# Kernel tuning notes

Measured on AMD Instinct MI355X. Metric: run time of the kernel, lower is better.

Reference implementation:

```python
import jax, jax.numpy as jnp
import numpy as np

B, S, HID = 2, 2048, 2304
H, KVH, D = 8, 4, 256          # query heads, kv heads, head_dim
N_REP = H // KVH
SCALE = 256.0 ** -0.5          # query_pre_attn_scalar ** -0.5
SOFTCAP = 50.0
ROPE_THETA = 10000.0
NEG = -1e9


def setup_inputs() -> dict:
    key = jax.random.key(0)
    k1, k2, k3, k4, k5 = jax.random.split(key, 5)
    hidden_states = jax.random.normal(k1, (B, S, HID), dtype=jnp.float32)
    # RoPE cos/sin tables, shape [B, S, D]
    inv_freq = 1.0 / (ROPE_THETA ** (jnp.arange(0, D, 2, dtype=jnp.float32) / D))
    pos = jnp.arange(S, dtype=jnp.float32)
    freqs = pos[:, None] * inv_freq[None, :]            # [S, D/2]
    emb = jnp.concatenate([freqs, freqs], axis=-1)      # [S, D]
    cos = jnp.broadcast_to(jnp.cos(emb)[None], (B, S, D))
    sin = jnp.broadcast_to(jnp.sin(emb)[None], (B, S, D))
    # additive causal mask [B, 1, S, S] (sliding_window=4096 > S, so pure causal)
    idx = jnp.arange(S)
    causal = idx[None, :] <= idx[:, None]
    attention_mask = jnp.broadcast_to(
        jnp.where(causal, 0.0, NEG).astype(jnp.float32)[None, None], (B, 1, S, S))
    # projection weights (lecun-normal-ish scale), no bias (attention_bias=False)
    Wq = jax.random.normal(k2, (HID, H * D), dtype=jnp.float32) / np.sqrt(HID)
    Wk = jax.random.normal(k3, (HID, KVH * D), dtype=jnp.float32) / np.sqrt(HID)
    Wv = jax.random.normal(k4, (HID, KVH * D), dtype=jnp.float32) / np.sqrt(HID)
    Wo = jax.random.normal(k5, (H * D, HID), dtype=jnp.float32) / np.sqrt(H * D)
    return {"hidden_states": hidden_states, "cos": cos, "sin": sin,
            "attention_mask": attention_mask,
            "Wq": Wq, "Wk": Wk, "Wv": Wv, "Wo": Wo}


def _rotate_half(x):
    half = x.shape[-1] // 2
    return jnp.concatenate([-x[..., half:], x[..., :half]], axis=-1)


def reference(hidden_states, cos, sin, attention_mask, Wq, Wk, Wv, Wo):
    b, s, _ = hidden_states.shape
    q = (hidden_states @ Wq).reshape(b, s, H, D).transpose(0, 2, 1, 3)    # [B,H,S,D]
    k = (hidden_states @ Wk).reshape(b, s, KVH, D).transpose(0, 2, 1, 3)  # [B,KVH,S,D]
    v = (hidden_states @ Wv).reshape(b, s, KVH, D).transpose(0, 2, 1, 3)
    c = cos[:, None]  # [B,1,S,D] broadcast over heads (unsqueeze_dim=1)
    sn = sin[:, None]
    q = q * c + _rotate_half(q) * sn
    k = k * c + _rotate_half(k) * sn
    # GQA: repeat kv heads (interleave, matching repeat_kv tile+reshape)
    k = jnp.repeat(k, N_REP, axis=1)
    v = jnp.repeat(v, N_REP, axis=1)
    w = jnp.einsum('bhqd,bhkd->bhqk', q, k) * SCALE
    w = jnp.tanh(w / SOFTCAP) * SOFTCAP                  # logit softcapping
    w = w + attention_mask[:, :, :, :s]
    w = jax.nn.softmax(w.astype(jnp.float32), axis=-1).astype(q.dtype)
    out = jnp.einsum('bhqk,bhkd->bhqd', w, v)
    out = out.transpose(0, 2, 1, 3).reshape(b, s, H * D)
    return out @ Wo
```

## Files before the change

### kernel.cpp

```cpp
#include <hip/hip_runtime.h>

typedef unsigned short u16;
typedef __attribute__((ext_vector_type(8))) short short8;
typedef __attribute__((ext_vector_type(4))) float f32x4;

constexpr int B_ = 2;
constexpr int H_ = 8;
constexpr int KVH_ = 4;
constexpr int S_ = 2048;
constexpr int D_ = 256;
constexpr int HID_ = 2304;
constexpr int QKVN_ = 4096;
constexpr int AON_ = 2048;

__device__ __forceinline__ float b2f(u16 u) {
  union { float f; unsigned int i; } x; x.i = ((unsigned int)u) << 16; return x.f;
}
__device__ __forceinline__ u16 f2b(float f) {
  unsigned int x = __float_as_uint(f);
  unsigned int r = (x + 0x7fffu + ((x >> 16) & 1u)) >> 16;
  return (u16)r;
}

__global__ void cast_kernel(const float* __restrict__ in, u16* __restrict__ out) {
  size_t i = ((size_t)blockIdx.x * 256 + threadIdx.x) * 4;
  float4 v = *(const float4*)(in + i);
  unsigned int lo = (unsigned int)f2b(v.x) | ((unsigned int)f2b(v.y) << 16);
  unsigned int hi = (unsigned int)f2b(v.z) | ((unsigned int)f2b(v.w) << 16);
  uint2 o; o.x = lo; o.y = hi;
  *(uint2*)(out + i) = o;
}

__global__ void transpose_cast(const float* __restrict__ src, u16* __restrict__ dst,
                               int R, int C) {
  __shared__ float tile[64][65];
  int r0 = blockIdx.y * 64, c0 = blockIdx.x * 64;
  int t = threadIdx.x;
#pragma unroll
  for (int i = 0; i < 16; ++i) {
    int e = i * 256 + t;
    int r = e >> 6, c = e & 63;
    tile[r][c] = src[(size_t)(r0 + r) * C + (c0 + c)];
  }
  __syncthreads();
#pragma unroll
  for (int i = 0; i < 16; ++i) {
    int e = i * 256 + t;
    int orow = e >> 6, ocol = e & 63;
    dst[(size_t)(c0 + orow) * R + (r0 + ocol)] = f2b(tile[ocol][orow]);
  }
}

template <int OUTF32>
__global__ __launch_bounds__(256, 2) void gemm_bt(
    const u16* __restrict__ A, const u16* __restrict__ B, void* __restrict__ Cp,
    int M, int N, int K) {
  __shared__ u16 As[128 * 32];
  __shared__ u16 Bs[128 * 32];
  int m0 = blockIdx.y * 128, n0 = blockIdx.x * 128;
  int tid = threadIdx.x;
  int lane = tid & 63, wave = tid >> 6;
  int wy = wave >> 1, wx = wave & 1;
  int quad = lane >> 4, l16 = lane & 15;
  f32x4 acc[4][4] = {};
  for (int k0 = 0; k0 < K; k0 += 32) {
#pragma unroll
    for (int i = 0; i < 2; ++i) {
      int chunk = i * 256 + tid;
      int row = chunk >> 2, col = (chunk & 3) << 3;
      __builtin_amdgcn_global_load_lds(
          (const __attribute__((address_space(1))) void*)(A + (size_t)(m0 + row) * K + k0 + col),
          (__attribute__((address_space(3))) void*)(As + chunk * 8), 16, 0, 0);
    }
#pragma unroll
    for (int i = 0; i < 2; ++i) {
      int chunk = i * 256 + tid;
      int row = chunk >> 2, col = (chunk & 3) << 3;
      __builtin_amdgcn_global_load_lds(
          (const __attribute__((address_space(1))) void*)(B + (size_t)(n0 + row) * K + k0 + col),
          (__attribute__((address_space(3))) void*)(Bs + chunk * 8), 16, 0, 0);
    }
    __syncthreads();
    short8 af[4], bf[4];
#pragma unroll
    for (int mi = 0; mi < 4; ++mi)
      af[mi] = *(const short8*)(As + (wy * 64 + mi * 16 + l16) * 32 + quad * 8);
#pragma unroll
    for (int ni = 0; ni < 4; ++ni)
      bf[ni] = *(const short8*)(Bs + (wx * 64 + ni * 16 + l16) * 32 + quad * 8);
#pragma unroll
    for (int mi = 0; mi < 4; ++mi)
#pragma unroll
      for (int ni = 0; ni < 4; ++ni)
        acc[mi][ni] = __builtin_amdgcn_mfma_f32_16x16x32_bf16(af[mi], bf[ni], acc[mi][ni], 0, 0, 0);
    __syncthreads();
  }
#pragma unroll
  for (int mi = 0; mi < 4; ++mi) {
#pragma unroll
    for (int ni = 0; ni < 4; ++ni) {
#pragma unroll
      for (int r = 0; r < 4; ++r) {
        int row = m0 + wy * 64 + mi * 16 + quad * 4 + r;
        int col = n0 + wx * 64 + ni * 16 + l16;
        if (OUTF32)
          ((float*)Cp)[(size_t)row * N + col] = acc[mi][ni][r];
        else
          ((u16*)Cp)[(size_t)row * N + col] = f2b(acc[mi][ni][r]);
      }
    }
  }
}

__global__ void rope_kernel(const u16* __restrict__ qkv, const float* __restrict__ cs,
                            const float* __restrict__ sn, u16* __restrict__ Qr,
                            u16* __restrict__ Kr) {
  int row = blockIdx.x;
  int b = row >> 11, s = row & 2047;
  int d = threadIdx.x;
  const u16* qrow = qkv + (size_t)row * QKVN_;
  float c = cs[(size_t)row * D_ + d];
  float si = sn[(size_t)row * D_ + d];
  int dp = (d < 128) ? d + 128 : d - 128;
  float sgn = (d < 128) ? -1.f : 1.f;
#pragma unroll
  for (int h = 0; h < H_; ++h) {
    float v = b2f(qrow[h * D_ + d]);
    float p = sgn * b2f(qrow[h * D_ + dp]);
    Qr[((size_t)(b * H_ + h) * S_ + s) * D_ + d] = f2b(v * c + p * si);
  }
#pragma unroll
  for (int g = 0; g < KVH_; ++g) {
    float v = b2f(qrow[2048 + g * D_ + d]);
    float p = sgn * b2f(qrow[2048 + g * D_ + dp]);
    Kr[((size_t)(b * KVH_ + g) * S_ + s) * D_ + d] = f2b(v * c + p * si);
  }
}

__global__ void transpose_v(const u16* __restrict__ qkv, u16* __restrict__ Vt) {
  __shared__ u16 tile[64][72];
  int d0 = blockIdx.x * 64, s0 = blockIdx.y * 64, g = blockIdx.z;
  int b = g >> 2, kvh = g & 3;
  int t = threadIdx.x;
#pragma unroll
  for (int i = 0; i < 16; ++i) {
    int e = i * 256 + t;
    int r = e >> 6, c = e & 63;
    tile[r][c] = qkv[(size_t)(b * S_ + s0 + r) * QKVN_ + 3072 + kvh * D_ + d0 + c];
  }
  __syncthreads();
#pragma unroll
  for (int i = 0; i < 16; ++i) {
    int e = i * 256 + t;
    int orow = e >> 6, ocol = e & 63;
    Vt[((size_t)g * D_ + d0 + orow) * S_ + s0 + ocol] = tile[ocol][orow];
  }
}

__global__ __launch_bounds__(256, 2) void attn_kernel(
    const u16* __restrict__ Qr, const u16* __restrict__ Kr, const u16* __restrict__ Vt,
    u16* __restrict__ Ao) {
  __shared__ u16 Ks[32 * 256];
  __shared__ u16 Vs[256 * 32];
  __shared__ u16 Ps[4][16 * 40];
  int b = blockIdx.z;
  int qt = (b == 0) ? (31 - blockIdx.x) : blockIdx.x;
  int h = blockIdx.y;
  int kvh = h >> 1;
  int tid = threadIdx.x, wave = tid >> 6, lane = tid & 63;
  int quad = lane >> 4, l16 = lane & 15;
  int q0 = qt * 64;
  const u16* Qbase = Qr + ((size_t)(b * H_ + h) * S_ + q0 + wave * 16 + l16) * D_;
  short8 qf[8];
#pragma unroll
  for (int kk = 0; kk < 8; ++kk)
    qf[kk] = *(const short8*)(Qbase + kk * 32 + quad * 8);
  const u16* Kbase = Kr + (size_t)(b * KVH_ + kvh) * S_ * D_;
  const u16* Vbase = Vt + (size_t)(b * KVH_ + kvh) * D_ * S_;
  float l_r[4] = {0.f, 0.f, 0.f, 0.f};
  f32x4 o_acc[16] = {};
  int nkt = 2 * qt + 2;
  for (int kt = 0; kt < nkt; ++kt) {
    int k0 = kt * 32;
    __syncthreads();
#pragma unroll
    for (int i = 0; i < 4; ++i) {
      int p = i * 256 + tid;
      int s = p >> 5, pc = p & 31;
      int c = pc ^ (s & 7);
      __builtin_amdgcn_global_load_lds(
          (const __attribute__((address_space(1))) void*)(Kbase + (size_t)(k0 + s) * D_ + c * 8),
          (__attribute__((address_space(3))) void*)(Ks + p * 8), 16, 0, 0);
    }
#pragma unroll
    for (int i = 0; i < 4; ++i) {
      int p = i * 256 + tid;
      int d = p >> 2, ps = p & 3;
      int sl = ps ^ ((d >> 1) & 3);
      __builtin_amdgcn_global_load_lds(
          (const __attribute__((address_space(1))) void*)(Vbase + (size_t)d * S_ + k0 + sl * 8),
          (__attribute__((address_space(3))) void*)(Vs + p * 8), 16, 0, 0);
    }
    __syncthreads();
    f32x4 sacc[2] = {};
#pragma unroll
    for (int n = 0; n < 2; ++n) {
      int srow = n * 16 + l16;
      const u16* kb = Ks + srow * 256;
      int sw = l16 & 7;
#pragma unroll
      for (int kk = 0; kk < 8; ++kk) {
        int phys = (kk * 4 + quad) ^ sw;
        short8 bfr = *(const short8*)(kb + phys * 8);
        sacc[n] = __builtin_amdgcn_mfma_f32_16x16x32_bf16(qf[kk], bfr, sacc[n], 0, 0, 0);
      }
    }
    float rs[4] = {0.f, 0.f, 0.f, 0.f};
    bool full = (k0 + 31 <= q0 + wave * 16);
#pragma unroll
    for (int n = 0; n < 2; ++n) {
      int key = k0 + n * 16 + l16;
#pragma unroll
      for (int r = 0; r < 4; ++r) {
        float E = __expf(sacc[n][r] * 0.0025f);
        float ee = __expf(-100.0f * __frcp_rn(E + 1.0f));
        if (!full) {
          int qq = q0 + wave * 16 + quad * 4 + r;
          ee = (key <= qq) ? ee : 0.0f;
        }
        rs[r] += ee;
        Ps[wave][(quad * 4 + r) * 40 + n * 16 + l16] = f2b(ee);
      }
    }
#pragma unroll
    for (int off = 1; off < 16; off <<= 1)
#pragma unroll
      for (int r = 0; r < 4; ++r)
        rs[r] += __shfl_xor(rs[r], off, 64);
#pragma unroll
    for (int r = 0; r < 4; ++r) l_r[r] += rs[r];
    short8 pa = *(const short8*)(&Ps[wave][l16 * 40 + quad * 8]);
#pragma unroll
    for (int dt = 0; dt < 16; ++dt) {
      int d = dt * 16 + l16;
      int phys = quad ^ ((d >> 1) & 3);
      short8 vb = *(const short8*)(Vs + d * 32 + phys * 8);
      o_acc[dt] = __builtin_amdgcn_mfma_f32_16x16x32_bf16(pa, vb, o_acc[dt], 0, 0, 0);
    }
  }
#pragma unroll
  for (int r = 0; r < 4; ++r) l_r[r] = 1.0f / l_r[r];
#pragma unroll
  for (int dt = 0; dt < 16; ++dt)
#pragma unroll
    for (int r = 0; r < 4; ++r) {
      int row = b * S_ + q0 + wave * 16 + quad * 4 + r;
      int col = h * D_ + dt * 16 + l16;
      Ao[(size_t)row * AON_ + col] = f2b(o_acc[dt][r] * l_r[r]);
    }
}

extern "C" void kernel_launch(void* const* d_in, const int* in_sizes, int n_in,
                              void* d_out, int out_size, void* d_ws, size_t ws_size,
                              hipStream_t stream) {
  const float* hidden = (const float*)d_in[0];
  const float* cosp = (const float*)d_in[1];
  const float* sinp = (const float*)d_in[2];
  const float* Wq = (const float*)d_in[4];
  const float* Wk = (const float*)d_in[5];
  const float* Wv = (const float*)d_in[6];
  const float* Wo = (const float*)d_in[7];

  u16* hs  = (u16*)d_ws;
  u16* WT  = hs  + (size_t)4096 * HID_;
  u16* WoT = WT  + (size_t)4096 * HID_;
  u16* qkv = WoT + (size_t)HID_ * AON_;
  u16* Qr  = qkv + (size_t)4096 * QKVN_;
  u16* Kr  = Qr  + (size_t)B_ * H_ * S_ * D_;
  u16* Vt  = Kr  + (size_t)B_ * KVH_ * S_ * D_;
  u16* Ao  = Vt  + (size_t)B_ * KVH_ * S_ * D_;

  cast_kernel<<<9216, 256, 0, stream>>>(hidden, hs);
  transpose_cast<<<dim3(32, 36), 256, 0, stream>>>(Wq, WT, HID_, 2048);
  transpose_cast<<<dim3(16, 36), 256, 0, stream>>>(Wk, WT + (size_t)2048 * HID_, HID_, 1024);
  transpose_cast<<<dim3(16, 36), 256, 0, stream>>>(Wv, WT + (size_t)3072 * HID_, HID_, 1024);
  transpose_cast<<<dim3(36, 32), 256, 0, stream>>>(Wo, WoT, 2048, HID_);
  gemm_bt<0><<<dim3(32, 32), 256, 0, stream>>>(hs, WT, qkv, 4096, QKVN_, HID_);
  rope_kernel<<<4096, 256, 0, stream>>>(qkv, cosp, sinp, Qr, Kr);
  transpose_v<<<dim3(4, 32, 8), 256, 0, stream>>>(qkv, Vt);
  attn_kernel<<<dim3(32, 8, 2), 256, 0, stream>>>(Qr, Kr, Vt, Ao);
  gemm_bt<1><<<dim3(18, 32), 256, 0, stream>>>(Ao, WoT, d_out, 4096, HID_, 2048);
}
```

Before: 451.5 us.

## Double-buffer K/V LDS tiles and defer row-sum reduction to kernel end

The attention kernel now keeps two LDS buffers for K and V and issues the async global-to-LDS loads for the next key tile before computing on the current one. This overlaps memory latency with MFMA work and drops one barrier per iteration. The per-tile cross-lane shuffle reduction of the softmax row sums is replaced by per-lane partial sums reduced once after the loop. LDS use roughly doubles, which may limit occupancy at the requested two blocks per SM, and correctness relies on the trailing barrier ordering the buffer reuse.

```diff
diff --git a/kernel.cpp b/kernel.cpp
--- a/kernel.cpp
+++ b/kernel.cpp
@@ -160,8 +160,8 @@
 __global__ __launch_bounds__(256, 2) void attn_kernel(
     const u16* __restrict__ Qr, const u16* __restrict__ Kr, const u16* __restrict__ Vt,
     u16* __restrict__ Ao) {
-  __shared__ u16 Ks[32 * 256];
-  __shared__ u16 Vs[256 * 32];
+  __shared__ u16 Ks[2][32 * 256];
+  __shared__ u16 Vs[2][32 * 256];
   __shared__ u16 Ps[4][16 * 40];
   int b = blockIdx.z;
   int qt = (b == 0) ? (31 - blockIdx.x) : blockIdx.x;
@@ -177,36 +177,49 @@
     qf[kk] = *(const short8*)(Qbase + kk * 32 + quad * 8);
   const u16* Kbase = Kr + (size_t)(b * KVH_ + kvh) * S_ * D_;
   const u16* Vbase = Vt + (size_t)(b * KVH_ + kvh) * D_ * S_;
-  float l_r[4] = {0.f, 0.f, 0.f, 0.f};
+  int ksrc_s[4], ksrc_c[4], vsrc_d[4], vsrc_s[4];
+#pragma unroll
+  for (int i = 0; i < 4; ++i) {
+    int p = i * 256 + tid;
+    ksrc_s[i] = p >> 5;
+    ksrc_c[i] = (p & 31) ^ ((p >> 5) & 7);
+    vsrc_d[i] = p >> 2;
+    vsrc_s[i] = (p & 3) ^ ((p >> 3) & 3);
+  }
+  float lp[4] = {0.f, 0.f, 0.f, 0.f};
   f32x4 o_acc[16] = {};
   int nkt = 2 * qt + 2;
+
+#define STAGE(KT, BUF)                                                                   \
+  {                                                                                      \
+    int k0s = (KT) * 32;                                                                 \
+    _Pragma("unroll") for (int i = 0; i < 4; ++i) {                                      \
+      int p = i * 256 + tid;                                                             \
+      __builtin_amdgcn_global_load_lds(                                                  \
+          (const __attribute__((address_space(1))) void*)(Kbase +                        \
+              (size_t)(k0s + ksrc_s[i]) * D_ + ksrc_c[i] * 8),                           \
+          (__attribute__((address_space(3))) void*)(&Ks[BUF][0] + p * 8), 16, 0, 0);     \
+    }                                                                                    \
+    _Pragma("unroll") for (int i = 0; i < 4; ++i) {                                      \
+      int p = i * 256 + tid;                                                             \
+      __builtin_amdgcn_global_load_lds(                                                  \
+          (const __attribute__((address_space(1))) void*)(Vbase +                        \
+              (size_t)vsrc_d[i] * S_ + k0s + vsrc_s[i] * 8),                             \
+          (__attribute__((address_space(3))) void*)(&Vs[BUF][0] + p * 8), 16, 0, 0);     \
+    }                                                                                    \
+  }
+
+  STAGE(0, 0);
+  __syncthreads();
   for (int kt = 0; kt < nkt; ++kt) {
     int k0 = kt * 32;
-    __syncthreads();
-#pragma unroll
-    for (int i = 0; i < 4; ++i) {
-      int p = i * 256 + tid;
-      int s = p >> 5, pc = p & 31;
-      int c = pc ^ (s & 7);
-      __builtin_amdgcn_global_load_lds(
-          (const __attribute__((address_space(1))) void*)(Kbase + (size_t)(k0 + s) * D_ + c * 8),
-          (__attribute__((address_space(3))) void*)(Ks + p * 8), 16, 0, 0);
-    }
-#pragma unroll
-    for (int i = 0; i < 4; ++i) {
-      int p = i * 256 + tid;
-      int d = p >> 2, ps = p & 3;
-      int sl = ps ^ ((d >> 1) & 3);
-      __builtin_amdgcn_global_load_lds(
-          (const __attribute__((address_space(1))) void*)(Vbase + (size_t)d * S_ + k0 + sl * 8),
-          (__attribute__((address_space(3))) void*)(Vs + p * 8), 16, 0, 0);
-    }
-    __syncthreads();
+    int cur = kt & 1;
+    if (kt + 1 < nkt) STAGE(kt + 1, cur ^ 1);
     f32x4 sacc[2] = {};
 #pragma unroll
     for (int n = 0; n < 2; ++n) {
       int srow = n * 16 + l16;
-      const u16* kb = Ks + srow * 256;
+      const u16* kb = &Ks[cur][0] + srow * 256;
       int sw = l16 & 7;
 #pragma unroll
       for (int kk = 0; kk < 8; ++kk) {
@@ -215,7 +228,6 @@
         sacc[n] = __builtin_amdgcn_mfma_f32_16x16x32_bf16(qf[kk], bfr, sacc[n], 0, 0, 0);
       }
     }
-    float rs[4] = {0.f, 0.f, 0.f, 0.f};
     bool full = (k0 + 31 <= q0 + wave * 16);
 #pragma unroll
     for (int n = 0; n < 2; ++n) {
@@ -228,35 +240,35 @@
           int qq = q0 + wave * 16 + quad * 4 + r;
           ee = (key <= qq) ? ee : 0.0f;
         }
-        rs[r] += ee;
+        lp[r] += ee;
         Ps[wave][(quad * 4 + r) * 40 + n * 16 + l16] = f2b(ee);
       }
     }
-#pragma unroll
-    for (int off = 1; off < 16; off <<= 1)
-#pragma unroll
-      for (int r = 0; r < 4; ++r)
-        rs[r] += __shfl_xor(rs[r], off, 64);
-#pragma unroll
-    for (int r = 0; r < 4; ++r) l_r[r] += rs[r];
     short8 pa = *(const short8*)(&Ps[wave][l16 * 40 + quad * 8]);
 #pragma unroll
     for (int dt = 0; dt < 16; ++dt) {
       int d = dt * 16 + l16;
       int phys = quad ^ ((d >> 1) & 3);
-      short8 vb = *(const short8*)(Vs + d * 32 + phys * 8);
+      short8 vb = *(const short8*)(&Vs[cur][0] + d * 32 + phys * 8);
       o_acc[dt] = __builtin_amdgcn_mfma_f32_16x16x32_bf16(pa, vb, o_acc[dt], 0, 0, 0);
     }
-  }
-#pragma unroll
-  for (int r = 0; r < 4; ++r) l_r[r] = 1.0f / l_r[r];
+    __syncthreads();
+  }
+#undef STAGE
+#pragma unroll
+  for (int off = 1; off < 16; off <<= 1)
+#pragma unroll
+    for (int r = 0; r < 4; ++r)
+      lp[r] += __shfl_xor(lp[r], off, 64);
+#pragma unroll
+  for (int r = 0; r < 4; ++r) lp[r] = 1.0f / lp[r];
 #pragma unroll
   for (int dt = 0; dt < 16; ++dt)
 #pragma unroll
     for (int r = 0; r < 4; ++r) {
       int row = b * S_ + q0 + wave * 16 + quad * 4 + r;
       int col = h * D_ + dt * 16 + l16;
-      Ao[(size_t)row * AON_ + col] = f2b(o_acc[dt][r] * l_r[r]);
+      Ao[(size_t)row * AON_ + col] = f2b(o_acc[dt][r] * lp[r]);
     }
 }
 
```

Result: faster. 441.2 us (-2.3%).
